# Performance work log

Measured on AMD Instinct MI355X. Metric: run time of the kernel, lower is better.

## Reference

```python
import jax, jax.numpy as jnp
import numpy as np

N_QUBITS = 4
LAYERS = 2
NUM_HEADS = 8
EMBED = 32
DK = EMBED // NUM_HEADS  # == N_QUBITS
B, S = 32, 4096


def _ry(t):
    c, s = jnp.cos(t / 2), jnp.sin(t / 2)
    m = jnp.stack([jnp.stack([c, -s], -1), jnp.stack([s, c], -1)], -2)
    return m.astype(jnp.complex64)


def _rx(t):
    c = jnp.cos(t / 2).astype(jnp.complex64)
    s = (-1j) * jnp.sin(t / 2).astype(jnp.complex64)
    return jnp.stack([jnp.stack([c, s], -1), jnp.stack([s, c], -1)], -2)


def _rz(t):
    em = jnp.exp(-0.5j * t.astype(jnp.complex64))
    ep = jnp.conj(em)
    z = jnp.zeros_like(em)
    return jnp.stack([jnp.stack([em, z], -1), jnp.stack([z, ep], -1)], -2)


def _apply_1q(state, U, w, n):
    # state: (B, 2**n); wire 0 is the most-significant bit (PennyLane convention)
    s = state.reshape(-1, 2 ** w, 2, 2 ** (n - 1 - w))
    if U.ndim == 2:  # shared gate
        s = jnp.einsum('ij,bpjq->bpiq', U, s)
    else:  # per-token gate, U: (B,2,2)
        s = jnp.einsum('bij,bpjq->bpiq', U, s)
    return s.reshape(-1, 2 ** n)


def _cnot(state, c, t, n):
    s = state.reshape((-1,) + (2,) * n)
    c_ax, t_ax = 1 + c, 1 + t
    s0 = jax.lax.slice_in_dim(s, 0, 1, axis=c_ax)
    s1 = jax.lax.slice_in_dim(s, 1, 2, axis=c_ax)
    s1 = jnp.flip(s1, axis=t_ax)  # X on target where control == 1
    s = jnp.concatenate([s0, s1], axis=c_ax)
    return s.reshape(-1, 2 ** n)


def _z_expvals(state, n):
    p = jnp.abs(state) ** 2  # (B, 2**n)
    outs = []
    for i in range(n):
        pr = p.reshape(-1, 2 ** i, 2, 2 ** (n - 1 - i))
        outs.append(pr[:, :, 0, :].sum((1, 2)) - pr[:, :, 1, :].sum((1, 2)))
    return jnp.stack(outs, -1)  # (B, n)


def _head_fwd(x_h, p_h):
    # x_h: (BT, n_qubits) angles, p_h: (layers, n_qubits, 3)
    n, L = N_QUBITS, LAYERS
    bt = x_h.shape[0]
    state = jnp.zeros((bt, 2 ** n), jnp.complex64).at[:, 0].set(1.0)
    for i in range(n):
        state = _apply_1q(state, _ry(x_h[:, i]), i, n)
    for l in range(L):
        for i in range(n):
            state = _apply_1q(state, _rx(p_h[l, i, 0]), i, n)
            state = _apply_1q(state, _ry(p_h[l, i, 1]), i, n)
            state = _apply_1q(state, _rz(p_h[l, i, 2]), i, n)
        for i in range(n - 1):
            state = _cnot(state, i, i + 1, n)
        state = _cnot(state, n - 1, 0, n)
    return _z_expvals(state, n)


def setup_inputs() -> dict:
    key = jax.random.key(0)
    k1, k2, k3, k4 = jax.random.split(key, 4)
    x = jax.random.normal(k1, (B, S, EMBED), jnp.float32)
    params = jax.random.normal(k2, (NUM_HEADS, LAYERS, N_QUBITS, 3), jnp.float32)
    fan_in = NUM_HEADS * N_QUBITS
    bound = 1.0 / np.sqrt(fan_in)
    W_out = jax.random.uniform(k3, (EMBED, fan_in), jnp.float32, -bound, bound)
    b_out = jax.random.uniform(k4, (EMBED,), jnp.float32, -bound, bound)
    return {'x': x, 'params': params, 'W_out': W_out, 'b_out': b_out}


def reference(x, params, W_out, b_out):
    b, s, e = x.shape
    xh = x.reshape(b, s, NUM_HEADS, DK)
    xh = jnp.moveaxis(xh, 2, 0).reshape(NUM_HEADS, b * s, DK)  # (H, BT, d_k)
    ang = xh[:, :, :N_QUBITS]  # angles fed into RY embedding
    ev = jax.vmap(_head_fwd)(ang, params)  # (H, BT, n_qubits)
    concat = jnp.moveaxis(ev, 0, 1).reshape(b, s, NUM_HEADS * N_QUBITS)
    return concat @ W_out.T + b_out
```

## Files before the change

kernel.cpp:

```cpp
#include <hip/hip_runtime.h>
#include <math.h>

#define NQ   4
#define NH   8
#define NL   2
#define DIM  16
#define EMB  32
#define TPB  64
#define EVP  33
#define EHS  328

using cfloat = const __attribute__((address_space(4))) float;
__device__ __forceinline__ cfloat* cptr(const float* p) {
    return (cfloat*)(unsigned long long)p;
}

__global__ void build_unitaries_kernel(const float* __restrict__ params,
                                       float* __restrict__ Uws) {
    int tid = threadIdx.x;
    int h   = tid >> 4;
    int col = tid & 15;

    float re[DIM], im[DIM];
#pragma unroll
    for (int j = 0; j < DIM; ++j) { re[j] = (j == col) ? 1.f : 0.f; im[j] = 0.f; }

#pragma unroll
    for (int l = 0; l < NL; ++l) {
#pragma unroll
        for (int q = 0; q < NQ; ++q) {
            const float* p = params + ((h * NL + l) * NQ + q) * 3;
            const int m = 1 << (3 - q);
            {
                float s, c; __sincosf(0.5f * p[0], &s, &c);
#pragma unroll
                for (int j = 0; j < DIM; ++j) {
                    if (j & m) continue;
                    const int j1 = j | m;
                    float r0 = re[j], i0 = im[j], r1 = re[j1], i1 = im[j1];
                    re[j]  = c * r0 + s * i1;
                    im[j]  = c * i0 - s * r1;
                    re[j1] = s * i0 + c * r1;
                    im[j1] = -s * r0 + c * i1;
                }
            }
            {
                float s, c; __sincosf(0.5f * p[1], &s, &c);
#pragma unroll
                for (int j = 0; j < DIM; ++j) {
                    if (j & m) continue;
                    const int j1 = j | m;
                    float r0 = re[j], i0 = im[j], r1 = re[j1], i1 = im[j1];
                    re[j]  = c * r0 - s * r1;
                    im[j]  = c * i0 - s * i1;
                    re[j1] = s * r0 + c * r1;
                    im[j1] = s * i0 + c * i1;
                }
            }
            {
                float s, c; __sincosf(0.5f * p[2], &s, &c);
#pragma unroll
                for (int j = 0; j < DIM; ++j) {
                    if (j & m) continue;
                    const int j1 = j | m;
                    float r0 = re[j], i0 = im[j], r1 = re[j1], i1 = im[j1];
                    re[j]  = c * r0 + s * i0;
                    im[j]  = c * i0 - s * r0;
                    re[j1] = c * r1 - s * i1;
                    im[j1] = c * i1 + s * r1;
                }
            }
        }
#pragma unroll
        for (int e = 0; e < NQ; ++e) {
            const int cm = 1 << (3 - e), tm = 1 << (3 - ((e + 1) & 3));
#pragma unroll
            for (int j = 0; j < DIM; ++j) {
                if ((j & cm) && !(j & tm)) {
                    const int j1 = j | tm;
                    float tr = re[j]; re[j] = re[j1]; re[j1] = tr;
                    float ti = im[j]; im[j] = im[j1]; im[j1] = ti;
                }
            }
        }
    }
#pragma unroll
    for (int j = 0; j < DIM; ++j) {
        Uws[(h * DIM + j) * DIM + col]        = re[j];
        Uws[2048 + (h * DIM + j) * DIM + col] = im[j];
    }
}

__global__ void build_E_kernel(const float* __restrict__ Uws,
                               float* __restrict__ Ews) {
    const int h   = blockIdx.x;
    const int tid = threadIdx.x;
    __shared__ float Urs[256], Uis[256];
    if (tid < 256) {
        Urs[tid] = Uws[h * 256 + tid];
        Uis[tid] = Uws[2048 + h * 256 + tid];
    }
    __syncthreads();
    if (tid >= 324) return;

    const int q  = tid / 81;
    const int ab = tid % 81;
    const int a = ab / 9, b = ab % 9;
    const int t0 = a / 3, t1 = a % 3, t2 = b / 3, t3 = b % 3;

    float Sv[16];
#pragma unroll
    for (int m = 0; m < 16; ++m) Sv[m] = 0.f;

    for (int c = 0; c < 16; ++c) {
        const int o0 = (c >> 3) & 1, o1 = (c >> 2) & 1;
        const int o2 = (c >> 1) & 1, o3 = c & 1;
        float sg = 1.f;
        const int bk0 = (t0 == 2) ? (1 - o0) : o0; if (t0 == 1 && o0) sg = -sg;
        const int bk1 = (t1 == 2) ? (1 - o1) : o1; if (t1 == 1 && o1) sg = -sg;
        const int bk2 = (t2 == 2) ? (1 - o2) : o2; if (t2 == 1 && o2) sg = -sg;
        const int bk3 = (t3 == 2) ? (1 - o3) : o3; if (t3 == 1 && o3) sg = -sg;
        const int j = (o0 << 3) | (o1 << 2) | (o2 << 1) | o3;
        const int k = (bk0 << 3) | (bk1 << 2) | (bk2 << 1) | bk3;
#pragma unroll
        for (int m = 0; m < 16; ++m) {
            const float v = Urs[m * 16 + j] * Urs[m * 16 + k]
                          + Uis[m * 16 + j] * Uis[m * 16 + k];
            Sv[m] = fmaf(sg, v, Sv[m]);
        }
    }
    float acc = 0.f;
#pragma unroll
    for (int m = 0; m < 16; ++m)
        acc += ((m >> (3 - q)) & 1) ? -Sv[m] : Sv[m];

    Ews[h * EHS + tid] = acc * 0.0625f;
}

__global__ __launch_bounds__(512, 4)
void qmha_kernel(const float* __restrict__ x,
                 const float* __restrict__ Ews,
                 const float* __restrict__ W,
                 const float* __restrict__ bvec,
                 float* __restrict__ out) {
    __shared__ float evs[TPB * EVP];

    const int tid  = threadIdx.x;
    const int tok0 = blockIdx.x * TPB;
    const int lane = tid & 63;

    {
        const int h = __builtin_amdgcn_readfirstlane(tid >> 6);
        const int tok = tok0 + lane;

        const float4 xa = *(const float4*)(x + (size_t)tok * EMB + h * NQ);
        float C0, S0, C1, S1, C2, S2, C3, S3;
        __sincosf(xa.x, &S0, &C0);
        __sincosf(xa.y, &S1, &C1);
        __sincosf(xa.z, &S2, &C2);
        __sincosf(xa.w, &S3, &C3);

        float m01[9], m23[9];
        m01[0] = 1.f; m01[1] = C1;      m01[2] = S1;
        m01[3] = C0;  m01[4] = C0 * C1; m01[5] = C0 * S1;
        m01[6] = S0;  m01[7] = S0 * C1; m01[8] = S0 * S1;
        m23[0] = 1.f; m23[1] = C3;      m23[2] = S3;
        m23[3] = C2;  m23[4] = C2 * C3; m23[5] = C2 * S3;
        m23[6] = S2;  m23[7] = S2 * C3; m23[8] = S2 * S3;

        cfloat* E = cptr(Ews + h * EHS);

#pragma unroll
        for (int q = 0; q < NQ; ++q) {
            float acc = 0.f;
#pragma unroll
            for (int a = 0; a < 9; ++a) {
                float inner = 0.f;
#pragma unroll
                for (int b = 0; b < 9; ++b)
                    inner = fmaf(E[q * 81 + a * 9 + b], m23[b], inner);
                acc = fmaf(m01[a], inner, acc);
            }
            evs[lane * EVP + h * 4 + q] = acc;
        }
    }
    __syncthreads();

    {
        const int w  = __builtin_amdgcn_readfirstlane(tid >> 6);
        const int e0 = w * 4;

        cfloat* Wr = cptr(W);
        cfloat* bc = cptr(bvec);

        float o0 = bc[e0 + 0], o1 = bc[e0 + 1], o2 = bc[e0 + 2], o3 = bc[e0 + 3];
#pragma unroll
        for (int k = 0; k < EMB; ++k) {
            const float evk = evs[lane * EVP + k];
            o0 = fmaf(Wr[(e0 + 0) * EMB + k], evk, o0);
            o1 = fmaf(Wr[(e0 + 1) * EMB + k], evk, o1);
            o2 = fmaf(Wr[(e0 + 2) * EMB + k], evk, o2);
            o3 = fmaf(Wr[(e0 + 3) * EMB + k], evk, o3);
        }
        float4 v; v.x = o0; v.y = o1; v.z = o2; v.w = o3;
        *(float4*)(out + (size_t)(tok0 + lane) * EMB + e0) = v;
    }
}

extern "C" void kernel_launch(void* const* d_in, const int* in_sizes, int n_in,
                              void* d_out, int out_size, void* d_ws, size_t ws_size,
                              hipStream_t stream) {
    const float* x      = (const float*)d_in[0];
    const float* params = (const float*)d_in[1];
    const float* W_out  = (const float*)d_in[2];
    const float* b_out  = (const float*)d_in[3];
    float*       out    = (float*)d_out;
    float*       Uws    = (float*)d_ws;
    float*       Ews    = (float*)d_ws + 4096;

    const int ntok = in_sizes[0] / EMB;

    hipLaunchKernelGGL(build_unitaries_kernel, dim3(1), dim3(128), 0, stream,
                       params, Uws);
    hipLaunchKernelGGL(build_E_kernel, dim3(NH), dim3(384), 0, stream,
                       Uws, Ews);
    hipLaunchKernelGGL(qmha_kernel, dim3(ntok / TPB), dim3(512), 0, stream,
                       x, Ews, W_out, b_out, out);
}
```

Measured before the change: 100.2 us.

## Fuse setup kernels, pack E and W for vector loads and packed FMAs

Merges the unitary-building and E-building kernels into one setup kernel, so there is one fewer launch and no global round trip for U. It also re-lays E as interleaved q-quads and W as pair-interleaved columns so the main kernel can use 16-byte loads and two-wide packed FMAs. The main kernel drops the address-space(4) constant pointer trick and the occupancy hint in launch bounds. Loads may now go through vector memory instead of scalar loads, and register pressure may rise.

```diff
diff --git a/kernel.cpp b/kernel.cpp
--- a/kernel.cpp
+++ b/kernel.cpp
@@ -7,100 +7,101 @@
 #define DIM  16
 #define EMB  32
 #define TPB  64
-#define EVP  33
-#define EHS  328
-
-using cfloat = const __attribute__((address_space(4))) float;
-__device__ __forceinline__ cfloat* cptr(const float* p) {
-    return (cfloat*)(unsigned long long)p;
-}
-
-__global__ void build_unitaries_kernel(const float* __restrict__ params,
-                                       float* __restrict__ Uws) {
-    int tid = threadIdx.x;
-    int h   = tid >> 4;
-    int col = tid & 15;
-
-    float re[DIM], im[DIM];
-#pragma unroll
-    for (int j = 0; j < DIM; ++j) { re[j] = (j == col) ? 1.f : 0.f; im[j] = 0.f; }
-
-#pragma unroll
-    for (int l = 0; l < NL; ++l) {
-#pragma unroll
-        for (int q = 0; q < NQ; ++q) {
-            const float* p = params + ((h * NL + l) * NQ + q) * 3;
-            const int m = 1 << (3 - q);
-            {
-                float s, c; __sincosf(0.5f * p[0], &s, &c);
-#pragma unroll
-                for (int j = 0; j < DIM; ++j) {
-                    if (j & m) continue;
-                    const int j1 = j | m;
-                    float r0 = re[j], i0 = im[j], r1 = re[j1], i1 = im[j1];
-                    re[j]  = c * r0 + s * i1;
-                    im[j]  = c * i0 - s * r1;
-                    re[j1] = s * i0 + c * r1;
-                    im[j1] = -s * r0 + c * i1;
-                }
-            }
-            {
-                float s, c; __sincosf(0.5f * p[1], &s, &c);
-#pragma unroll
-                for (int j = 0; j < DIM; ++j) {
-                    if (j & m) continue;
-                    const int j1 = j | m;
-                    float r0 = re[j], i0 = im[j], r1 = re[j1], i1 = im[j1];
-                    re[j]  = c * r0 - s * r1;
-                    im[j]  = c * i0 - s * i1;
-                    re[j1] = s * r0 + c * r1;
-                    im[j1] = s * i0 + c * i1;
-                }
-            }
-            {
-                float s, c; __sincosf(0.5f * p[2], &s, &c);
-#pragma unroll
-                for (int j = 0; j < DIM; ++j) {
-                    if (j & m) continue;
-                    const int j1 = j | m;
-                    float r0 = re[j], i0 = im[j], r1 = re[j1], i1 = im[j1];
-                    re[j]  = c * r0 + s * i0;
-                    im[j]  = c * i0 - s * r0;
-                    re[j1] = c * r1 - s * i1;
-                    im[j1] = c * i1 + s * r1;
-                }
-            }
-        }
-#pragma unroll
-        for (int e = 0; e < NQ; ++e) {
-            const int cm = 1 << (3 - e), tm = 1 << (3 - ((e + 1) & 3));
-#pragma unroll
-            for (int j = 0; j < DIM; ++j) {
-                if ((j & cm) && !(j & tm)) {
-                    const int j1 = j | tm;
-                    float tr = re[j]; re[j] = re[j1]; re[j1] = tr;
-                    float ti = im[j]; im[j] = im[j1]; im[j1] = ti;
-                }
-            }
-        }
-    }
-#pragma unroll
-    for (int j = 0; j < DIM; ++j) {
-        Uws[(h * DIM + j) * DIM + col]        = re[j];
-        Uws[2048 + (h * DIM + j) * DIM + col] = im[j];
-    }
-}
-
-__global__ void build_E_kernel(const float* __restrict__ Uws,
-                               float* __restrict__ Ews) {
+#define EVP  34
+#define EH   324
+#define WPK_OFF (NH * EH)
+
+typedef float v2f __attribute__((ext_vector_type(2)));
+typedef float v4f __attribute__((ext_vector_type(4)));
+
+__global__ void setup_kernel(const float* __restrict__ params,
+                             const float* __restrict__ W,
+                             float* __restrict__ ws) {
+    __shared__ float Urs[256], Uis[256];
     const int h   = blockIdx.x;
     const int tid = threadIdx.x;
-    __shared__ float Urs[256], Uis[256];
-    if (tid < 256) {
-        Urs[tid] = Uws[h * 256 + tid];
-        Uis[tid] = Uws[2048 + h * 256 + tid];
+
+    if (tid < 16) {
+        const int col = tid;
+        float re[DIM], im[DIM];
+#pragma unroll
+        for (int j = 0; j < DIM; ++j) { re[j] = (j == col) ? 1.f : 0.f; im[j] = 0.f; }
+
+#pragma unroll
+        for (int l = 0; l < NL; ++l) {
+#pragma unroll
+            for (int q = 0; q < NQ; ++q) {
+                const float* p = params + ((h * NL + l) * NQ + q) * 3;
+                const int m = 1 << (3 - q);
+                {
+                    float s, c; __sincosf(0.5f * p[0], &s, &c);
+#pragma unroll
+                    for (int j = 0; j < DIM; ++j) {
+                        if (j & m) continue;
+                        const int j1 = j | m;
+                        float r0 = re[j], i0 = im[j], r1 = re[j1], i1 = im[j1];
+                        re[j]  = c * r0 + s * i1;
+                        im[j]  = c * i0 - s * r1;
+                        re[j1] = s * i0 + c * r1;
+                        im[j1] = -s * r0 + c * i1;
+                    }
+                }
+                {
+                    float s, c; __sincosf(0.5f * p[1], &s, &c);
+#pragma unroll
+                    for (int j = 0; j < DIM; ++j) {
+                        if (j & m) continue;
+                        const int j1 = j | m;
+                        float r0 = re[j], i0 = im[j], r1 = re[j1], i1 = im[j1];
+                        re[j]  = c * r0 - s * r1;
+                        im[j]  = c * i0 - s * i1;
+                        re[j1] = s * r0 + c * r1;
+                        im[j1] = s * i0 + c * i1;
+                    }
+                }
+                {
+                    float s, c; __sincosf(0.5f * p[2], &s, &c);
+#pragma unroll
+                    for (int j = 0; j < DIM; ++j) {
+                        if (j & m) continue;
+                        const int j1 = j | m;
+                        float r0 = re[j], i0 = im[j], r1 = re[j1], i1 = im[j1];
+                        re[j]  = c * r0 + s * i0;
+                        im[j]  = c * i0 - s * r0;
+                        re[j1] = c * r1 - s * i1;
+                        im[j1] = c * i1 + s * r1;
+                    }
+                }
+            }
+#pragma unroll
+            for (int e = 0; e < NQ; ++e) {
+                const int cm = 1 << (3 - e), tm = 1 << (3 - ((e + 1) & 3));
+#pragma unroll
+                for (int j = 0; j < DIM; ++j) {
+                    if ((j & cm) && !(j & tm)) {
+                        const int j1 = j | tm;
+                        float tr = re[j]; re[j] = re[j1]; re[j1] = tr;
+                        float ti = im[j]; im[j] = im[j1]; im[j1] = ti;
+                    }
+                }
+            }
+        }
+#pragma unroll
+        for (int j = 0; j < DIM; ++j) {
+            Urs[j * 16 + col] = re[j];
+            Uis[j * 16 + col] = im[j];
+        }
+    } else if (tid >= 64 && tid < 128) {
+        const int i  = tid - 64;
+        const int ep = 2 * h + (i >> 5);
+        const int k  = i & 31;
+        float2 v;
+        v.x = W[(2 * ep) * EMB + k];
+        v.y = W[(2 * ep + 1) * EMB + k];
+        *(float2*)(ws + WPK_OFF + (ep * EMB + k) * 2) = v;
     }
     __syncthreads();
+
     if (tid >= 324) return;
 
     const int q  = tid / 81;
@@ -134,13 +135,12 @@
     for (int m = 0; m < 16; ++m)
         acc += ((m >> (3 - q)) & 1) ? -Sv[m] : Sv[m];
 
-    Ews[h * EHS + tid] = acc * 0.0625f;
+    ws[h * EH + ab * 4 + q] = acc * 0.0625f;
 }
 
-__global__ __launch_bounds__(512, 4)
+__global__ __launch_bounds__(512)
 void qmha_kernel(const float* __restrict__ x,
-                 const float* __restrict__ Ews,
-                 const float* __restrict__ W,
+                 const float* __restrict__ ws,
                  const float* __restrict__ bvec,
                  float* __restrict__ out) {
     __shared__ float evs[TPB * EVP];
@@ -168,42 +168,55 @@
         m23[3] = C2;  m23[4] = C2 * C3; m23[5] = C2 * S3;
         m23[6] = S2;  m23[7] = S2 * C3; m23[8] = S2 * S3;
 
-        cfloat* E = cptr(Ews + h * EHS);
-
-#pragma unroll
-        for (int q = 0; q < NQ; ++q) {
-            float acc = 0.f;
-#pragma unroll
-            for (int a = 0; a < 9; ++a) {
-                float inner = 0.f;
-#pragma unroll
-                for (int b = 0; b < 9; ++b)
-                    inner = fmaf(E[q * 81 + a * 9 + b], m23[b], inner);
-                acc = fmaf(m01[a], inner, acc);
+        const v4f* __restrict__ E4 = (const v4f*)(ws + h * EH);
+
+        v2f ev01 = {0.f, 0.f}, ev23 = {0.f, 0.f};
+#pragma unroll
+        for (int a = 0; a < 9; ++a) {
+            v2f i01 = {0.f, 0.f}, i23 = {0.f, 0.f};
+#pragma unroll
+            for (int b = 0; b < 9; ++b) {
+                const v4f e = E4[a * 9 + b];
+                const v2f mb = {m23[b], m23[b]};
+                i01 = __builtin_elementwise_fma(__builtin_shufflevector(e, e, 0, 1), mb, i01);
+                i23 = __builtin_elementwise_fma(__builtin_shufflevector(e, e, 2, 3), mb, i23);
             }
-            evs[lane * EVP + h * 4 + q] = acc;
-        }
+            const v2f ma = {m01[a], m01[a]};
+            ev01 = __builtin_elementwise_fma(ma, i01, ev01);
+            ev23 = __builtin_elementwise_fma(ma, i23, ev23);
+        }
+
+        evs[lane * EVP + h * 4 + 0] = ev01.x;
+        evs[lane * EVP + h * 4 + 1] = ev01.y;
+        evs[lane * EVP + h * 4 + 2] = ev23.x;
+        evs[lane * EVP + h * 4 + 3] = ev23.y;
     }
     __syncthreads();
 
     {
-        const int w  = __builtin_amdgcn_readfirstlane(tid >> 6);
-        const int e0 = w * 4;
-
-        cfloat* Wr = cptr(W);
-        cfloat* bc = cptr(bvec);
-
-        float o0 = bc[e0 + 0], o1 = bc[e0 + 1], o2 = bc[e0 + 2], o3 = bc[e0 + 3];
-#pragma unroll
-        for (int k = 0; k < EMB; ++k) {
-            const float evk = evs[lane * EVP + k];
-            o0 = fmaf(Wr[(e0 + 0) * EMB + k], evk, o0);
-            o1 = fmaf(Wr[(e0 + 1) * EMB + k], evk, o1);
-            o2 = fmaf(Wr[(e0 + 2) * EMB + k], evk, o2);
-            o3 = fmaf(Wr[(e0 + 3) * EMB + k], evk, o3);
-        }
-        float4 v; v.x = o0; v.y = o1; v.z = o2; v.w = o3;
-        *(float4*)(out + (size_t)(tok0 + lane) * EMB + e0) = v;
+        const int w   = __builtin_amdgcn_readfirstlane(tid >> 6);
+        const int e0  = w * 4;
+        const int ep0 = w * 2;
+
+        const v4f* __restrict__ Wp0 = (const v4f*)(ws + WPK_OFF + (ep0 + 0) * 64);
+        const v4f* __restrict__ Wp1 = (const v4f*)(ws + WPK_OFF + (ep0 + 1) * 64);
+
+        v2f o01 = {bvec[e0 + 0], bvec[e0 + 1]};
+        v2f o23 = {bvec[e0 + 2], bvec[e0 + 3]};
+#pragma unroll
+        for (int kk = 0; kk < 16; ++kk) {
+            const v4f A = Wp0[kk];
+            const v4f B = Wp1[kk];
+            const v2f ev2 = *(const v2f*)(evs + lane * EVP + 2 * kk);
+            const v2f ek0 = {ev2.x, ev2.x};
+            const v2f ek1 = {ev2.y, ev2.y};
+            o01 = __builtin_elementwise_fma(__builtin_shufflevector(A, A, 0, 1), ek0, o01);
+            o01 = __builtin_elementwise_fma(__builtin_shufflevector(A, A, 2, 3), ek1, o01);
+            o23 = __builtin_elementwise_fma(__builtin_shufflevector(B, B, 0, 1), ek0, o23);
+            o23 = __builtin_elementwise_fma(__builtin_shufflevector(B, B, 2, 3), ek1, o23);
+        }
+        v4f v = {o01.x, o01.y, o23.x, o23.y};
+        *(v4f*)(out + (size_t)(tok0 + lane) * EMB + e0) = v;
     }
 }
 
@@ -215,15 +228,12 @@
     const float* W_out  = (const float*)d_in[2];
     const float* b_out  = (const float*)d_in[3];
     float*       out    = (float*)d_out;
-    float*       Uws    = (float*)d_ws;
-    float*       Ews    = (float*)d_ws + 4096;
+    float*       ws     = (float*)d_ws;
 
     const int ntok = in_sizes[0] / EMB;
 
-    hipLaunchKernelGGL(build_unitaries_kernel, dim3(1), dim3(128), 0, stream,
-                       params, Uws);
-    hipLaunchKernelGGL(build_E_kernel, dim3(NH), dim3(384), 0, stream,
-                       Uws, Ews);
+    hipLaunchKernelGGL(setup_kernel, dim3(NH), dim3(384), 0, stream,
+                       params, W_out, ws);
     hipLaunchKernelGGL(qmha_kernel, dim3(ntok / TPB), dim3(512), 0, stream,
-                       x, Ews, W_out, b_out, out);
+                       x, ws, b_out, out);
 }
```

Result: faster. 96.68 us (-3.5%).
